# Kernel tuning notes

Measured on AMD Instinct MI355X. Metric: run time of the kernel, lower is better.

## Reference

```python
import jax, jax.numpy as jnp
import numpy as np

HID = 768        # config.hidden_size
MM_HID = 1024    # config.mmodal_hidden_size
N_Q = 64         # config.num_queries
WIN = 512        # config.window_size
LN_EPS = 1e-5


def _window_starts(m, n, w):
    # mirrors split_tensor's start-index logic (static, computed in numpy)
    step = max(1, (m - w) // (n - 1))
    starts = []
    for i in range(n):
        s = i * step
        if s + w > m:
            s = m - w
        starts.append(s)
    return np.asarray(starts, dtype=np.int32)


def layernorm(x, g, b):
    mu = jnp.mean(x, axis=-1, keepdims=True)
    var = jnp.var(x, axis=-1, keepdims=True)
    return (x - mu) * jax.lax.rsqrt(var + LN_EPS) * g + b


def setup_inputs() -> dict:
    key = jax.random.key(0)
    ks = jax.random.split(key, 12)
    b, m, li = 4, 8192, 77
    s = lambda fan_in: 1.0 / np.sqrt(fan_in)
    inp = {
        'x_mmodal': jax.random.normal(ks[0], (b, m, MM_HID), jnp.float32),
        'inst_feats': jax.random.normal(ks[1], (b, li, HID), jnp.float32),
        'queries': jax.random.normal(ks[2], (1, N_Q, HID), jnp.float32),
        'W_proj': jax.random.normal(ks[3], (HID, HID), jnp.float32) * s(HID),
        'b_proj': jnp.zeros((HID,), jnp.float32),
        'W_kv_inst': jax.random.normal(ks[4], (HID, 2 * HID), jnp.float32) * s(HID),
        'b_kv_inst': jnp.zeros((2 * HID,), jnp.float32),
        'W_out_inst': jax.random.normal(ks[5], (HID, HID), jnp.float32) * s(HID),
        'b_out_inst': jnp.zeros((HID,), jnp.float32),
        'W_kv_mm': jax.random.normal(ks[6], (MM_HID, 2 * HID), jnp.float32) * s(MM_HID),
        'b_kv_mm': jnp.zeros((2 * HID,), jnp.float32),
        'W_out_mm': jax.random.normal(ks[7], (HID, HID), jnp.float32) * s(HID),
        'b_out_mm': jnp.zeros((HID,), jnp.float32),
        'ln_g': jnp.ones((HID,), jnp.float32),
        'ln_b': jnp.zeros((HID,), jnp.float32),
    }
    return inp


def reference(x_mmodal, inst_feats, queries, W_proj, b_proj, W_kv_inst,
              b_kv_inst, W_out_inst, b_out_inst, W_kv_mm, b_kv_mm,
              W_out_mm, b_out_mm, ln_g, ln_b):
    b = x_mmodal.shape[0]
    scale = 1.0 / jnp.sqrt(jnp.asarray(HID, x_mmodal.dtype))

    # ---- dense cross-attention over instruction features ----
    inst = inst_feats @ W_proj + b_proj                      # (b, li, d)
    k, v = jnp.split(inst @ W_kv_inst + b_kv_inst, 2, axis=-1)
    k = layernorm(k, ln_g, ln_b)
    v = layernorm(v, ln_g, ln_b)
    q = jnp.broadcast_to(queries, (b, N_Q, HID))
    attn = jnp.einsum('bnd,bmd->bnm', q, k) * scale
    attn = jax.nn.softmax(attn, axis=-1)
    q = jnp.einsum('bnm,bmd->bnd', attn, v)
    q = layernorm(q @ W_out_inst + b_out_inst, ln_g, ln_b)

    # ---- swin-style overlapping windowed cross-attention over mmodal ----
    k, v = jnp.split(x_mmodal @ W_kv_mm + b_kv_mm, 2, axis=-1)
    k = layernorm(k, ln_g, ln_b)
    v = layernorm(v, ln_g, ln_b)
    m = k.shape[1]
    starts = _window_starts(m, N_Q, WIN)                     # (n,)
    idx = jnp.asarray(starts[:, None] + np.arange(WIN))      # (n, w)
    kw = k[:, idx]                                           # (b, n, w, d)
    vw = v[:, idx]                                           # (b, n, w, d)
    a = jnp.einsum('bnd,bnwd->bnw', q, kw) * scale
    a = jax.nn.softmax(a, axis=-1)
    out = jnp.einsum('bnw,bnwd->bnd', a, vw)
    out = layernorm(out @ W_out_mm + b_out_mm, ln_g, ln_b)
    return out
```

## Files before the change

### kernel.cpp

```cpp
#include <hip/hip_runtime.h>

#define HIDDEN 768
#define NQ 64
#define WINSZ 512
#define MSEQ 8192
#define BATCH 4
#define LI 77
#define MMHID 1024
#define LN_EPS 1e-5f
#define SCALE_QK 0.03608439182435161f

typedef __attribute__((ext_vector_type(8))) short short8v;
typedef __attribute__((ext_vector_type(4))) float f32x4;
typedef __attribute__((ext_vector_type(8))) unsigned short u16x8;

#define AS1 __attribute__((address_space(1)))
#define AS3 __attribute__((address_space(3)))

__device__ inline unsigned short f2bf(float f) {
    unsigned u = __float_as_uint(f);
    u += 0x7fffu + ((u >> 16) & 1u);
    return (unsigned short)(u >> 16);
}
__device__ inline float bf2f(unsigned short h) {
    return __uint_as_float(((unsigned)h) << 16);
}

__device__ inline void block_reduce2_256(float& s1, float& s2, float* sm) {
    #pragma unroll
    for (int o = 32; o; o >>= 1) { s1 += __shfl_down(s1, o); s2 += __shfl_down(s2, o); }
    int lane = threadIdx.x & 63, w = threadIdx.x >> 6;
    __syncthreads();
    if (lane == 0) { sm[w] = s1; sm[4 + w] = s2; }
    __syncthreads();
    s1 = sm[0] + sm[1] + sm[2] + sm[3];
    s2 = sm[4] + sm[5] + sm[6] + sm[7];
}

__global__ __launch_bounds__(256) void cvt_kernel(const float* __restrict__ in,
                                                  unsigned short* __restrict__ out, int n8) {
    int i = blockIdx.x * 256 + threadIdx.x;
    if (i >= n8) return;
    const float4* p = (const float4*)(in + (size_t)i * 8);
    float4 a = p[0], b = p[1];
    u16x8 o;
    o[0] = f2bf(a.x); o[1] = f2bf(a.y); o[2] = f2bf(a.z); o[3] = f2bf(a.w);
    o[4] = f2bf(b.x); o[5] = f2bf(b.y); o[6] = f2bf(b.z); o[7] = f2bf(b.w);
    *(u16x8*)(out + (size_t)i * 8) = o;
}

__global__ __launch_bounds__(256) void cvt_q_kernel(const float* __restrict__ q2,
                                                    const float* __restrict__ g,
                                                    const float* __restrict__ bb,
                                                    unsigned short* __restrict__ q2bf,
                                                    float* __restrict__ qgsum) {
    int blk = blockIdx.x;
    int b = blk >> 7, r = blk & 127;
    int t = threadIdx.x;
    __shared__ float sm[8];
    unsigned short* orow = q2bf + (size_t)blk * HIDDEN;
    if (r >= 64) {
        orow[t] = 0; orow[t + 256] = 0; orow[t + 512] = 0;
        return;
    }
    const float* qrow = q2 + ((size_t)(b * 64 + r)) * HIDDEN;
    float y0 = qrow[t], y1 = qrow[t + 256], y2 = qrow[t + 512];
    float s = y0 + y1 + y2, s2 = y0 * y0 + y1 * y1 + y2 * y2;
    block_reduce2_256(s, s2, sm);
    float mu = s * (1.f / 768.f);
    float var = s2 * (1.f / 768.f) - mu * mu;
    float inv = rsqrtf(var + LN_EPS);
    float qw0 = (y0 - mu) * inv * g[t]       + bb[t];
    float qw1 = (y1 - mu) * inv * g[t + 256] + bb[t + 256];
    float qw2 = (y2 - mu) * inv * g[t + 512] + bb[t + 512];
    float v0 = qw0 * g[t]       * SCALE_QK;
    float v1 = qw1 * g[t + 256] * SCALE_QK;
    float v2 = qw2 * g[t + 512] * SCALE_QK;
    orow[t] = f2bf(v0); orow[t + 256] = f2bf(v1); orow[t + 512] = f2bf(v2);
    float qs = v0 + v1 + v2, dummy = 0.f;
    block_reduce2_256(qs, dummy, sm);
    if (t == 0) qgsum[b * 64 + r] = qs;
}

struct PrepJobs {
    const float* W[5];
    unsigned short* Wt[5];
    int D[5];
    int C[5];
    const float* inst_in;
    unsigned short* inst_out;
    int n8_valid;
    int n8_total;
};
__global__ __launch_bounds__(256) void prep_kernel(PrepJobs tw) {
    int z = blockIdx.z;
    if (z == 5) {
        int flat = blockIdx.y * gridDim.x + blockIdx.x;
        int i = flat * 256 + threadIdx.x;
        if (i >= tw.n8_total) return;
        u16x8 o = {};
        if (i < tw.n8_valid) {
            const float4* p = (const float4*)(tw.inst_in + (size_t)i * 8);
            float4 a = p[0], b = p[1];
            o[0] = f2bf(a.x); o[1] = f2bf(a.y); o[2] = f2bf(a.z); o[3] = f2bf(a.w);
            o[4] = f2bf(b.x); o[5] = f2bf(b.y); o[6] = f2bf(b.z); o[7] = f2bf(b.w);
        }
        *(u16x8*)(tw.inst_out + (size_t)i * 8) = o;
        return;
    }
    int C = tw.C[z], D = tw.D[z];
    int n0 = blockIdx.x * 32, k0 = blockIdx.y * 32;
    if (n0 >= C || k0 >= D) return;
    const float* W = tw.W[z];
    unsigned short* Wt = tw.Wt[z];
    __shared__ float tile[32][33];
    int tx = threadIdx.x & 31, ty = (threadIdx.x >> 5);
    #pragma unroll
    for (int i = 0; i < 32; i += 8)
        tile[ty + i][tx] = W[(size_t)(k0 + ty + i) * C + n0 + tx];
    __syncthreads();
    #pragma unroll
    for (int i = 0; i < 32; i += 8)
        Wt[(size_t)(n0 + ty + i) * D + k0 + tx] = f2bf(tile[tx][ty + i]);
}

#define GM 32768
#define GN 1536
#define GK 1024

__global__ __launch_bounds__(256) void gemm_kv_kernel(const unsigned short* __restrict__ A,
                                                      const unsigned short* __restrict__ Bt,
                                                      const float* __restrict__ bias,
                                                      unsigned short* __restrict__ C) {
    __shared__ unsigned short sA[128 * 64];
    __shared__ unsigned short sB[128 * 64];

    int nwg = gridDim.x;
    int bid = blockIdx.x;
    int wg = bid;
    if ((nwg & 7) == 0) { int cpx = nwg >> 3; wg = (bid & 7) * cpx + (bid >> 3); }
    int bm = wg / (GN / 128), bn = wg % (GN / 128);
    int row0 = bm * 128, col0 = bn * 128;

    int tid = threadIdx.x;
    int lane = tid & 63, wid = tid >> 6;
    int wr = wid >> 1, wc = wid & 1;

    f32x4 acc[4][4] = {};

    int rS[4], cS[4];
    #pragma unroll
    for (int i = 0; i < 4; i++) {
        int ch = wid * 4 + i;
        int r = ch * 8 + (lane >> 3);
        rS[i] = r;
        cS[i] = ((lane & 7) ^ (r & 7)) << 3;
    }

    for (int k0 = 0; k0 < GK; k0 += 64) {
        #pragma unroll
        for (int i = 0; i < 4; i++) {
            int ch = wid * 4 + i;
            const unsigned short* ga = A + (size_t)(row0 + rS[i]) * GK + k0 + cS[i];
            __builtin_amdgcn_global_load_lds((const AS1 unsigned int*)ga,
                                             (AS3 unsigned int*)&sA[ch * 512], 16, 0, 0);
            const unsigned short* gb = Bt + (size_t)(col0 + rS[i]) * GK + k0 + cS[i];
            __builtin_amdgcn_global_load_lds((const AS1 unsigned int*)gb,
                                             (AS3 unsigned int*)&sB[ch * 512], 16, 0, 0);
        }
        __syncthreads();

        #pragma unroll
        for (int kk = 0; kk < 64; kk += 32) {
            int ko = (kk + ((lane >> 4) << 3)) * 2;
            short8v af[4], bf[4];
            #pragma unroll
            for (int m = 0; m < 4; m++) {
                int r = wr * 64 + m * 16 + (lane & 15);
                int addr = r * 128 + (ko ^ ((r & 7) << 4));
                af[m] = *(const short8v*)((const char*)sA + addr);
            }
            #pragma unroll
            for (int n = 0; n < 4; n++) {
                int r = wc * 64 + n * 16 + (lane & 15);
                int addr = r * 128 + (ko ^ ((r & 7) << 4));
                bf[n] = *(const short8v*)((const char*)sB + addr);
            }
            #pragma unroll
            for (int m = 0; m < 4; m++)
                #pragma unroll
                for (int n = 0; n < 4; n++)
                    acc[m][n] = __builtin_amdgcn_mfma_f32_16x16x32_bf16(af[m], bf[n], acc[m][n], 0, 0, 0);
        }
        __syncthreads();
    }

    int crow = (lane >> 4) * 4;
    int ccol = lane & 15;
    #pragma unroll
    for (int m = 0; m < 4; m++) {
        #pragma unroll
        for (int n = 0; n < 4; n++) {
            int gc = col0 + wc * 64 + n * 16 + ccol;
            float bv = bias[gc];
            #pragma unroll
            for (int j = 0; j < 4; j++) {
                int gr = row0 + wr * 64 + m * 16 + crow + j;
                C[(size_t)gr * GN + gc] = f2bf(acc[m][n][j] + bv);
            }
        }
    }
}

__global__ __launch_bounds__(256) void stats_kernel(const unsigned short* __restrict__ kv,
                                                    float2* __restrict__ stats) {
    int rh = blockIdx.x;
    const unsigned short* p = kv + (size_t)rh * 768;
    int t = threadIdx.x;
    float x0 = bf2f(p[t]), x1 = bf2f(p[t + 256]), x2 = bf2f(p[t + 512]);
    float s = x0 + x1 + x2, s2 = x0 * x0 + x1 * x1 + x2 * x2;
    __shared__ float sm[8];
    block_reduce2_256(s, s2, sm);
    if (t == 0) {
        float mu = s * (1.f / 768.f);
        float var = s2 * (1.f / 768.f) - mu * mu;
        float inv = rsqrtf(var + LN_EPS);
        stats[rh] = make_float2(mu * inv, inv);
    }
}

template <int TK, bool OUT_BF16>
__global__ __launch_bounds__(256) void gemm_tile_kernel(const unsigned short* __restrict__ A,
                                                        const unsigned short* __restrict__ Bt,
                                                        const float* __restrict__ bias,
                                                        void* __restrict__ Cout, int N) {
    __shared__ unsigned short sA[128 * 64];
    __shared__ unsigned short sB[128 * 64];

    int row0 = blockIdx.x * 128, col0 = blockIdx.y * 128;
    int tid = threadIdx.x;
    int lane = tid & 63, wid = tid >> 6;
    int wr = wid >> 1, wc = wid & 1;

    f32x4 acc[4][4] = {};

    int rS[4], cS[4];
    #pragma unroll
    for (int i = 0; i < 4; i++) {
        int ch = wid * 4 + i;
        int r = ch * 8 + (lane >> 3);
        rS[i] = r;
        cS[i] = ((lane & 7) ^ (r & 7)) << 3;
    }

    for (int k0 = 0; k0 < TK; k0 += 64) {
        #pragma unroll
        for (int i = 0; i < 4; i++) {
            int ch = wid * 4 + i;
            const unsigned short* ga = A + (size_t)(row0 + rS[i]) * TK + k0 + cS[i];
            __builtin_amdgcn_global_load_lds((const AS1 unsigned int*)ga,
                                             (AS3 unsigned int*)&sA[ch * 512], 16, 0, 0);
            const unsigned short* gb = Bt + (size_t)(col0 + rS[i]) * TK + k0 + cS[i];
            __builtin_amdgcn_global_load_lds((const AS1 unsigned int*)gb,
                                             (AS3 unsigned int*)&sB[ch * 512], 16, 0, 0);
        }
        __syncthreads();

        #pragma unroll
        for (int kk = 0; kk < 64; kk += 32) {
            int ko = (kk + ((lane >> 4) << 3)) * 2;
            short8v af[4], bf[4];
            #pragma unroll
            for (int m = 0; m < 4; m++) {
                int r = wr * 64 + m * 16 + (lane & 15);
                int addr = r * 128 + (ko ^ ((r & 7) << 4));
                af[m] = *(const short8v*)((const char*)sA + addr);
            }
            #pragma unroll
            for (int n = 0; n < 4; n++) {
                int r = wc * 64 + n * 16 + (lane & 15);
                int addr = r * 128 + (ko ^ ((r & 7) << 4));
                bf[n] = *(const short8v*)((const char*)sB + addr);
            }
            #pragma unroll
            for (int m = 0; m < 4; m++)
                #pragma unroll
                for (int n = 0; n < 4; n++)
                    acc[m][n] = __builtin_amdgcn_mfma_f32_16x16x32_bf16(af[m], bf[n], acc[m][n], 0, 0, 0);
        }
        __syncthreads();
    }

    int crow = (lane >> 4) * 4;
    int ccol = lane & 15;
    #pragma unroll
    for (int m = 0; m < 4; m++) {
        #pragma unroll
        for (int n = 0; n < 4; n++) {
            int gc = col0 + wc * 64 + n * 16 + ccol;
            float bv = bias[gc];
            #pragma unroll
            for (int j = 0; j < 4; j++) {
                int gr = row0 + wr * 64 + m * 16 + crow + j;
                float v = acc[m][n][j] + bv;
                if (OUT_BF16) ((unsigned short*)Cout)[(size_t)gr * N + gc] = f2bf(v);
                else          ((float*)Cout)[(size_t)gr * N + gc] = v;
            }
        }
    }
}

__global__ __launch_bounds__(256) void gemm_scores_kernel(const unsigned short* __restrict__ Aall,
                                                          const unsigned short* __restrict__ kv,
                                                          float* __restrict__ scores) {
    __shared__ unsigned short sA[128 * 64];
    __shared__ unsigned short sB[128 * 64];

    int b = blockIdx.y;
    int col0 = blockIdx.x * 128;
    const unsigned short* A = Aall + (size_t)b * 128 * HIDDEN;
    const unsigned short* Bt = kv + (size_t)b * MSEQ * 1536;

    int tid = threadIdx.x;
    int lane = tid & 63, wid = tid >> 6;
    int wr = wid >> 1, wc = wid & 1;

    f32x4 acc[4][4] = {};

    int rS[4], cS[4];
    #pragma unroll
    for (int i = 0; i < 4; i++) {
        int ch = wid * 4 + i;
        int r = ch * 8 + (lane >> 3);
        rS[i] = r;
        cS[i] = ((lane & 7) ^ (r & 7)) << 3;
    }

    for (int k0 = 0; k0 < HIDDEN; k0 += 64) {
        #pragma unroll
        for (int i = 0; i < 4; i++) {
            int ch = wid * 4 + i;
            const unsigned short* ga = A + (size_t)rS[i] * HIDDEN + k0 + cS[i];
            __builtin_amdgcn_global_load_lds((const AS1 unsigned int*)ga,
                                             (AS3 unsigned int*)&sA[ch * 512], 16, 0, 0);
            const unsigned short* gb = Bt + (size_t)(col0 + rS[i]) * 1536 + k0 + cS[i];
            __builtin_amdgcn_global_load_lds((const AS1 unsigned int*)gb,
                                             (AS3 unsigned int*)&sB[ch * 512], 16, 0, 0);
        }
        __syncthreads();

        #pragma unroll
        for (int kk = 0; kk < 64; kk += 32) {
            int ko = (kk + ((lane >> 4) << 3)) * 2;
            short8v af[4], bf[4];
            #pragma unroll
            for (int m = 0; m < 4; m++) {
                int r = wr * 64 + m * 16 + (lane & 15);
                int addr = r * 128 + (ko ^ ((r & 7) << 4));
                af[m] = *(const short8v*)((const char*)sA + addr);
            }
            #pragma unroll
            for (int n = 0; n < 4; n++) {
                int r = wc * 64 + n * 16 + (lane & 15);
                int addr = r * 128 + (ko ^ ((r & 7) << 4));
                bf[n] = *(const short8v*)((const char*)sB + addr);
            }
            #pragma unroll
            for (int m = 0; m < 4; m++)
                #pragma unroll
                for (int n = 0; n < 4; n++)
                    acc[m][n] = __builtin_amdgcn_mfma_f32_16x16x32_bf16(af[m], bf[n], acc[m][n], 0, 0, 0);
        }
        __syncthreads();
    }

    int crow = (lane >> 4) * 4;
    int ccol = lane & 15;
    #pragma unroll
    for (int m = 0; m < 4; m++) {
        #pragma unroll
        for (int n = 0; n < 4; n++) {
            int gc = col0 + wc * 64 + n * 16 + ccol;
            #pragma unroll
            for (int j = 0; j < 4; j++) {
                int gr = wr * 64 + m * 16 + crow + j;
                if (gr < 64)
                    scores[((size_t)(b * 64 + gr)) * MSEQ + gc] = acc[m][n][j];
            }
        }
    }
}

__global__ __launch_bounds__(512) void win_softmax_kernel(const float* __restrict__ scores,
                                                          const float2* __restrict__ stats,
                                                          const float* __restrict__ qgsum,
                                                          unsigned short* __restrict__ P_abs,
                                                          float* __restrict__ s2out) {
    int bidx = blockIdx.x;
    int b = bidx >> 6, n = bidx & 63;
    int step = (MSEQ - WINSZ) / (NQ - 1);
    int s = n * step;
    if (s + WINSZ > MSEQ) s = MSEQ - WINSZ;

    __shared__ float sm[8];
    int t = threadIdx.x, lane = t & 63, w = t >> 6;
    int r_abs = s + t;
    size_t rowidx = (size_t)b * MSEQ + r_abs;
    float2 stk = stats[rowidx * 2 + 0];
    float qg = qgsum[b * 64 + n];
    float a = stk.y * scores[((size_t)(b * 64 + n)) * MSEQ + r_abs] - qg * stk.x;

    float m = a;
    #pragma unroll
    for (int o = 32; o; o >>= 1) m = fmaxf(m, __shfl_down(m, o));
    if (lane == 0) sm[w] = m;
    __syncthreads();
    m = sm[0];
    #pragma unroll
    for (int i = 1; i < 8; i++) m = fmaxf(m, sm[i]);
    float e = expf(a - m);
    float ssum = e;
    #pragma unroll
    for (int o = 32; o; o >>= 1) ssum += __shfl_down(ssum, o);
    __syncthreads();
    if (lane == 0) sm[w] = ssum;
    __syncthreads();
    ssum = 0;
    #pragma unroll
    for (int i = 0; i < 8; i++) ssum += sm[i];
    float p = e / ssum;

    float2 stv = stats[rowidx * 2 + 1];
    float pt = p * stv.y;
    float s2p = p * stv.x;
    #pragma unroll
    for (int o = 32; o; o >>= 1) s2p += __shfl_down(s2p, o);
    __syncthreads();
    if (lane == 0) sm[w] = s2p;
    __syncthreads();
    if (t == 0) {
        float s2 = 0;
        #pragma unroll
        for (int i = 0; i < 8; i++) s2 += sm[i];
        s2out[b * 64 + n] = s2;
    }

    unsigned short* prow = P_abs + ((size_t)(b * 64 + n)) * MSEQ;
    for (int pos = t; pos < MSEQ; pos += 512)
        if (pos < s || pos >= s + WINSZ) prow[pos] = 0;
    prow[r_abs] = f2bf(pt);
}

__global__ __launch_bounds__(768) void pv_chunk_kernel(const unsigned short* __restrict__ P_abs,
                                                       const unsigned short* __restrict__ kv,
                                                       float* __restrict__ out_acc) {
    int b = blockIdx.y;
    int r0 = blockIdx.x * 64;
    int t = threadIdx.x;

    int n_lo = (r0 >= 512) ? ((r0 - 512) / 121 + 1) : 0;
    int n_hi = (r0 + 63) / 121;
    if (n_hi > 63) n_hi = 63;

    __shared__ float pw[5][64];
    if (t < 5 * 64) {
        int ni = t >> 6, r = t & 63;
        int n = n_lo + ni;
        float v = 0.f;
        if (n <= n_hi)
            v = bf2f(P_abs[((size_t)(b * 64 + n)) * MSEQ + r0 + r]);
        pw[ni][r] = v;
    }
    __syncthreads();

    const unsigned short* vbase = kv + ((size_t)(b * MSEQ + r0)) * 1536 + 768;
    float acc[5] = {};
    #pragma unroll 8
    for (int r = 0; r < 64; ++r) {
        float v = bf2f(vbase[(size_t)r * 1536 + t]);
        #pragma unroll
        for (int ni = 0; ni < 5; ni++) acc[ni] = fmaf(v, pw[ni][r], acc[ni]);
    }
    #pragma unroll
    for (int ni = 0; ni < 5; ni++) {
        int n = n_lo + ni;
        if (n <= n_hi)
            atomicAdd(&out_acc[((size_t)(b * 64 + n)) * HIDDEN + t], acc[ni]);
    }
}

__global__ __launch_bounds__(256) void out_affine_kernel(const float* __restrict__ o_acc,
                                                         const float* __restrict__ s2,
                                                         const float* __restrict__ g,
                                                         const float* __restrict__ bb,
                                                         unsigned short* __restrict__ a_bf) {
    int i = blockIdx.x * 256 + threadIdx.x;
    if (i >= BATCH * NQ * HIDDEN) return;
    int n = i / HIDDEN, d = i - n * HIDDEN;
    a_bf[i] = f2bf(g[d] * (o_acc[i] - s2[n]) + bb[d]);
}

__global__ __launch_bounds__(256) void ln_f32_rows(float* __restrict__ base,
                                                   const float* __restrict__ g,
                                                   const float* __restrict__ b) {
    int rh = blockIdx.x;
    float* p = base + (size_t)rh * 768;
    int t = threadIdx.x;
    float x0 = p[t], x1 = p[t + 256], x2 = p[t + 512];
    float s = x0 + x1 + x2, s2 = x0 * x0 + x1 * x1 + x2 * x2;
    __shared__ float sm[8];
    block_reduce2_256(s, s2, sm);
    float mu = s * (1.f / 768.f);
    float var = s2 * (1.f / 768.f) - mu * mu;
    float inv = rsqrtf(var + LN_EPS);
    p[t]       = (x0 - mu) * inv * g[t]       + b[t];
    p[t + 256] = (x1 - mu) * inv * g[t + 256] + b[t + 256];
    p[t + 512] = (x2 - mu) * inv * g[t + 512] + b[t + 512];
}

__global__ __launch_bounds__(256) void attn_inst_kernel(const float* __restrict__ queries,
                                                        const float* __restrict__ kv,
                                                        unsigned short* __restrict__ qatt) {
    int bidx = blockIdx.x;
    int b = bidx >> 6, n = bidx & 63;
    __shared__ float qs[HIDDEN];
    __shared__ float sc[LI], sc2[LI];
    int t = threadIdx.x, lane = t & 63, w = t >> 6;
    const float* q = queries + (size_t)n * HIDDEN;
    for (int d = t; d < HIDDEN; d += 256) qs[d] = q[d];
    __syncthreads();
    const float* kb = kv + (size_t)b * LI * 1536;
    for (int j = w; j < LI; j += 4) {
        const float* kr = kb + (size_t)j * 1536;
        float a = 0;
        #pragma unroll
        for (int i = 0; i < 12; i++) { int d = lane + i * 64; a = fmaf(kr[d], qs[d], a); }
        #pragma unroll
        for (int o = 32; o; o >>= 1) a += __shfl_down(a, o);
        if (lane == 0) sc[j] = a * SCALE_QK;
    }
    __syncthreads();
    float m = -1e30f;
    for (int j = 0; j < LI; j++) m = fmaxf(m, sc[j]);
    if (t < LI) sc2[t] = expf(sc[t] - m);
    __syncthreads();
    float s = 0;
    for (int j = 0; j < LI; j++) s += sc2[j];
    float inv = 1.f / s;
    float o0 = 0, o1 = 0, o2 = 0;
    for (int j = 0; j < LI; j++) {
        float p = sc2[j] * inv;
        const float* vr = kb + (size_t)j * 1536 + 768;
        o0 = fmaf(p, vr[t], o0);
        o1 = fmaf(p, vr[t + 256], o1);
        o2 = fmaf(p, vr[t + 512], o2);
    }
    unsigned short* orow = qatt + ((size_t)b * NQ + n) * HIDDEN;
    orow[t] = f2bf(o0); orow[t + 256] = f2bf(o1); orow[t + 512] = f2bf(o2);
}

extern "C" void kernel_launch(void* const* d_in, const int* in_sizes, int n_in,
                              void* d_out, int out_size, void* d_ws, size_t ws_size,
                              hipStream_t stream) {
    (void)in_sizes; (void)n_in; (void)out_size; (void)ws_size;
    const float* x_mm    = (const float*)d_in[0];
    const float* instf   = (const float*)d_in[1];
    const float* queries = (const float*)d_in[2];
    const float* W_proj  = (const float*)d_in[3];
    const float* b_proj  = (const float*)d_in[4];
    const float* W_kvi   = (const float*)d_in[5];
    const float* b_kvi   = (const float*)d_in[6];
    const float* W_oi    = (const float*)d_in[7];
    const float* b_oi    = (const float*)d_in[8];
    const float* W_kvm   = (const float*)d_in[9];
    const float* b_kvm   = (const float*)d_in[10];
    const float* W_om    = (const float*)d_in[11];
    const float* b_om    = (const float*)d_in[12];
    const float* ln_g    = (const float*)d_in[13];
    const float* ln_b    = (const float*)d_in[14];
    float* out = (float*)d_out;

    char* ws = (char*)d_ws;
    size_t off = 0;
    auto carve = [&](size_t bytes) -> char* {
        char* p = ws + off;
        off += (bytes + 255) & ~(size_t)255;
        return p;
    };
    unsigned short* x_bf   = (unsigned short*)carve((size_t)BATCH * MSEQ * MMHID * 2);
    unsigned short* wtm_bf = (unsigned short*)carve((size_t)2 * HIDDEN * MMHID * 2);
    unsigned short* kv_mm  = (unsigned short*)carve((size_t)BATCH * MSEQ * 2 * HIDDEN * 2);
    unsigned short* wp_bf  = (unsigned short*)carve((size_t)768 * 768 * 2);
    unsigned short* wkvi_bf= (unsigned short*)carve((size_t)1536 * 768 * 2);
    unsigned short* woi_bf = (unsigned short*)carve((size_t)768 * 768 * 2);
    unsigned short* wom_bf = (unsigned short*)carve((size_t)768 * 768 * 2);
    unsigned short* a1_bf  = (unsigned short*)carve((size_t)384 * 768 * 2);
    unsigned short* inst_bf= (unsigned short*)carve((size_t)384 * 768 * 2);
    float*          kv_inst= (float*)carve((size_t)384 * 1536 * 4);
    unsigned short* qatt_bf= (unsigned short*)carve((size_t)256 * 768 * 2);
    float*          q2     = (float*)carve((size_t)256 * 768 * 4);
    unsigned short* q2bf   = (unsigned short*)carve((size_t)BATCH * 128 * 768 * 2);
    float*          scores = (float*)carve((size_t)BATCH * 64 * MSEQ * 4);
    unsigned short* P_abs  = (unsigned short*)carve((size_t)BATCH * 64 * MSEQ * 2);
    float*          o_acc  = (float*)carve((size_t)BATCH * 64 * 768 * 4);
    unsigned short* a_bf   = (unsigned short*)carve((size_t)256 * 768 * 2);
    float2*         stats  = (float2*)carve((size_t)BATCH * MSEQ * 2 * sizeof(float2));
    float*          qgsum  = (float*)carve((size_t)256 * 4);
    float*          s2     = (float*)carve((size_t)256 * 4);

    PrepJobs tw;
    tw.W[0] = W_kvm;  tw.Wt[0] = wtm_bf;  tw.D[0] = 1024; tw.C[0] = 1536;
    tw.W[1] = W_proj; tw.Wt[1] = wp_bf;   tw.D[1] = 768;  tw.C[1] = 768;
    tw.W[2] = W_kvi;  tw.Wt[2] = wkvi_bf; tw.D[2] = 768;  tw.C[2] = 1536;
    tw.W[3] = W_oi;   tw.Wt[3] = woi_bf;  tw.D[3] = 768;  tw.C[3] = 768;
    tw.W[4] = W_om;   tw.Wt[4] = wom_bf;  tw.D[4] = 768;  tw.C[4] = 768;
    tw.inst_in = instf; tw.inst_out = a1_bf;
    tw.n8_valid = BATCH * LI * 768 / 8; tw.n8_total = 384 * 768 / 8;
    prep_kernel<<<dim3(48, 32, 6), 256, 0, stream>>>(tw);

    int n8 = BATCH * MSEQ * MMHID / 8;
    cvt_kernel<<<(n8 + 255) / 256, 256, 0, stream>>>(x_mm, x_bf, n8);
    gemm_kv_kernel<<<(GM / 128) * (GN / 128), 256, 0, stream>>>(x_bf, wtm_bf, b_kvm, kv_mm);
    stats_kernel<<<BATCH * MSEQ * 2, 256, 0, stream>>>(kv_mm, stats);

    gemm_tile_kernel<768, true><<<dim3(3, 6), 256, 0, stream>>>(a1_bf, wp_bf, b_proj, inst_bf, 768);
    gemm_tile_kernel<768, false><<<dim3(3, 12), 256, 0, stream>>>(inst_bf, wkvi_bf, b_kvi, kv_inst, 1536);
    ln_f32_rows<<<BATCH * LI * 2, 256, 0, stream>>>(kv_inst, ln_g, ln_b);
    attn_inst_kernel<<<BATCH * NQ, 256, 0, stream>>>(queries, kv_inst, qatt_bf);
    gemm_tile_kernel<768, false><<<dim3(2, 6), 256, 0, stream>>>(qatt_bf, woi_bf, b_oi, q2, 768);

    hipMemsetAsync(o_acc, 0, (size_t)BATCH * 64 * 768 * 4, stream);
    cvt_q_kernel<<<BATCH * 128, 256, 0, stream>>>(q2, ln_g, ln_b, q2bf, qgsum);
    gemm_scores_kernel<<<dim3(MSEQ / 128, BATCH), 256, 0, stream>>>(q2bf, kv_mm, scores);
    win_softmax_kernel<<<BATCH * NQ, 512, 0, stream>>>(scores, stats, qgsum, P_abs, s2);
    pv_chunk_kernel<<<dim3(MSEQ / 64, BATCH), 768, 0, stream>>>(P_abs, kv_mm, o_acc);
    out_affine_kernel<<<(BATCH * NQ * HIDDEN + 255) / 256, 256, 0, stream>>>(o_acc, s2, ln_g, ln_b, a_bf);

    gemm_tile_kernel<768, false><<<dim3(2, 6), 256, 0, stream>>>(a_bf, wom_bf, b_om, out, 768);
    ln_f32_rows<<<BATCH * NQ, 256, 0, stream>>>(out, ln_g, ln_b);
}
```

Baseline: 346.4 us.

## Use 256x256-tile double-buffered MFMA GEMM for multimodal KV projection

```diff
diff --git a/kernel.cpp b/kernel.cpp
--- a/kernel.cpp
+++ b/kernel.cpp
@@ -128,10 +128,116 @@
 #define GN 1536
 #define GK 1024
 
-__global__ __launch_bounds__(256) void gemm_kv_kernel(const unsigned short* __restrict__ A,
-                                                      const unsigned short* __restrict__ Bt,
-                                                      const float* __restrict__ bias,
-                                                      unsigned short* __restrict__ C) {
+__global__ __launch_bounds__(512, 2) void gemm_kv256_kernel(const unsigned short* __restrict__ A,
+                                                            const unsigned short* __restrict__ Bt,
+                                                            const float* __restrict__ bias,
+                                                            unsigned short* __restrict__ C) {
+    extern __shared__ char smem[];
+    unsigned short* sA = (unsigned short*)smem;
+    unsigned short* sB = (unsigned short*)(smem + 65536);
+
+    int nwg = gridDim.x;
+    int bid = blockIdx.x;
+    int wg = bid;
+    if ((nwg & 7) == 0) { int cpx = nwg >> 3; wg = (bid & 7) * cpx + (bid >> 3); }
+    int bm = wg / (GN / 256), bn = wg % (GN / 256);
+    int row0 = bm * 256, col0 = bn * 256;
+
+    int tid = threadIdx.x;
+    int lane = tid & 63, wid = tid >> 6;
+    int wm = wid >> 2, wn = wid & 3;
+
+    f32x4 acc[8][4] = {};
+
+    int rS[4], cS[4];
+    #pragma unroll
+    for (int i = 0; i < 4; i++) {
+        int ch = wid * 4 + i;
+        int r = ch * 8 + (lane >> 3);
+        rS[i] = r;
+        cS[i] = ((lane & 7) ^ (r & 7)) << 3;
+    }
+
+    auto STAGE = [&](int k0, int pbuf) {
+        unsigned short* dA = sA + pbuf * 16384;
+        unsigned short* dB = sB + pbuf * 16384;
+        #pragma unroll
+        for (int i = 0; i < 4; i++) {
+            int ch = wid * 4 + i;
+            const unsigned short* ga = A + (size_t)(row0 + rS[i]) * GK + k0 + cS[i];
+            __builtin_amdgcn_global_load_lds((const AS1 unsigned int*)ga,
+                                             (AS3 unsigned int*)&dA[ch * 512], 16, 0, 0);
+            const unsigned short* gb = Bt + (size_t)(col0 + rS[i]) * GK + k0 + cS[i];
+            __builtin_amdgcn_global_load_lds((const AS1 unsigned int*)gb,
+                                             (AS3 unsigned int*)&dB[ch * 512], 16, 0, 0);
+        }
+    };
+
+    STAGE(0, 0);
+    __syncthreads();
+
+    for (int kt = 0; kt < GK / 64; kt++) {
+        int cur = kt & 1;
+        if (kt < GK / 64 - 1) STAGE((kt + 1) * 64, cur ^ 1);
+
+        const char* lA = (const char*)(sA + cur * 16384);
+        const char* lB = (const char*)(sB + cur * 16384);
+
+        short8v bfr[4][2];
+        #pragma unroll
+        for (int n = 0; n < 4; n++)
+            #pragma unroll
+            for (int kk = 0; kk < 2; kk++) {
+                int r = wn * 64 + n * 16 + (lane & 15);
+                int ko = (kk * 32 + ((lane >> 4) << 3)) * 2;
+                bfr[n][kk] = *(const short8v*)(lB + r * 128 + (ko ^ ((r & 7) << 4)));
+            }
+        #pragma unroll
+        for (int p = 0; p < 4; p++) {
+            short8v afr[2][2];
+            #pragma unroll
+            for (int mf = 0; mf < 2; mf++)
+                #pragma unroll
+                for (int kk = 0; kk < 2; kk++) {
+                    int r = wm * 128 + (p * 2 + mf) * 16 + (lane & 15);
+                    int ko = (kk * 32 + ((lane >> 4) << 3)) * 2;
+                    afr[mf][kk] = *(const short8v*)(lA + r * 128 + (ko ^ ((r & 7) << 4)));
+                }
+            __builtin_amdgcn_s_setprio(1);
+            #pragma unroll
+            for (int mf = 0; mf < 2; mf++)
+                #pragma unroll
+                for (int n = 0; n < 4; n++)
+                    #pragma unroll
+                    for (int kk = 0; kk < 2; kk++)
+                        acc[p * 2 + mf][n] = __builtin_amdgcn_mfma_f32_16x16x32_bf16(
+                            afr[mf][kk], bfr[n][kk], acc[p * 2 + mf][n], 0, 0, 0);
+            __builtin_amdgcn_s_setprio(0);
+        }
+        __syncthreads();
+    }
+
+    int crow = (lane >> 4) * 4;
+    int ccol = lane & 15;
+    #pragma unroll
+    for (int m = 0; m < 8; m++) {
+        #pragma unroll
+        for (int n = 0; n < 4; n++) {
+            int gc = col0 + wn * 64 + n * 16 + ccol;
+            float bv = bias[gc];
+            #pragma unroll
+            for (int j = 0; j < 4; j++) {
+                int gr = row0 + wm * 128 + m * 16 + crow + j;
+                C[(size_t)gr * GN + gc] = f2bf(acc[m][n][j] + bv);
+            }
+        }
+    }
+}
+
+__global__ __launch_bounds__(256) void gemm_kv128_kernel(const unsigned short* __restrict__ A,
+                                                         const unsigned short* __restrict__ Bt,
+                                                         const float* __restrict__ bias,
+                                                         unsigned short* __restrict__ C) {
     __shared__ unsigned short sA[128 * 64];
     __shared__ unsigned short sB[128 * 64];
 
@@ -620,7 +726,13 @@
 
     int n8 = BATCH * MSEQ * MMHID / 8;
     cvt_kernel<<<(n8 + 255) / 256, 256, 0, stream>>>(x_mm, x_bf, n8);
-    gemm_kv_kernel<<<(GM / 128) * (GN / 128), 256, 0, stream>>>(x_bf, wtm_bf, b_kvm, kv_mm);
+    hipError_t attr_ok = hipFuncSetAttribute((const void*)gemm_kv256_kernel,
+                                             hipFuncAttributeMaxDynamicSharedMemorySize, 131072);
+    if (attr_ok == hipSuccess) {
+        gemm_kv256_kernel<<<(GM / 256) * (GN / 256), 512, 131072, stream>>>(x_bf, wtm_bf, b_kvm, kv_mm);
+    } else {
+        gemm_kv128_kernel<<<(GM / 128) * (GN / 128), 256, 0, stream>>>(x_bf, wtm_bf, b_kvm, kv_mm);
+    }
     stats_kernel<<<BATCH * MSEQ * 2, 256, 0, stream>>>(kv_mm, stats);
 
     gemm_tile_kernel<768, true><<<dim3(3, 6), 256, 0, stream>>>(a1_bf, wp_bf, b_proj, inst_bf, 768);
```

Result: faster. 320.3 us (-7.6%).

## Double-buffer KV GEMM with 256x128 tiles and fold o_acc zeroing into softmax

Applied to the files above, without the earlier changes.

```diff
diff --git a/kernel.cpp b/kernel.cpp
--- a/kernel.cpp
+++ b/kernel.cpp
@@ -128,69 +128,94 @@
 #define GN 1536
 #define GK 1024
 
-__global__ __launch_bounds__(256) void gemm_kv_kernel(const unsigned short* __restrict__ A,
-                                                      const unsigned short* __restrict__ Bt,
-                                                      const float* __restrict__ bias,
-                                                      unsigned short* __restrict__ C) {
-    __shared__ unsigned short sA[128 * 64];
-    __shared__ unsigned short sB[128 * 64];
+__global__ __launch_bounds__(256, 2) void gemm_kv_kernel(const unsigned short* __restrict__ A,
+                                                         const unsigned short* __restrict__ Bt,
+                                                         const float* __restrict__ bias,
+                                                         unsigned short* __restrict__ C) {
+    __shared__ unsigned short sA[2][256 * 32];
+    __shared__ unsigned short sB[2][128 * 32];
 
     int nwg = gridDim.x;
     int bid = blockIdx.x;
     int wg = bid;
     if ((nwg & 7) == 0) { int cpx = nwg >> 3; wg = (bid & 7) * cpx + (bid >> 3); }
     int bm = wg / (GN / 128), bn = wg % (GN / 128);
-    int row0 = bm * 128, col0 = bn * 128;
+    int row0 = bm * 256, col0 = bn * 128;
 
     int tid = threadIdx.x;
     int lane = tid & 63, wid = tid >> 6;
-    int wr = wid >> 1, wc = wid & 1;
-
-    f32x4 acc[4][4] = {};
-
-    int rS[4], cS[4];
+    int wm = wid >> 1, wn = wid & 1;
+
+    f32x4 acc[8][4] = {};
+
+    int rA[4], cA[4];
     #pragma unroll
     for (int i = 0; i < 4; i++) {
         int ch = wid * 4 + i;
-        int r = ch * 8 + (lane >> 3);
-        rS[i] = r;
-        cS[i] = ((lane & 7) ^ (r & 7)) << 3;
-    }
-
-    for (int k0 = 0; k0 < GK; k0 += 64) {
+        int r = ch * 16 + (lane >> 2);
+        rA[i] = r;
+        cA[i] = ((((lane & 3) * 16) ^ ((r & 6) << 3)) >> 1);
+    }
+    int rB[2], cB[2];
+    #pragma unroll
+    for (int i = 0; i < 2; i++) {
+        int ch = wid * 2 + i;
+        int r = ch * 16 + (lane >> 2);
+        rB[i] = r;
+        cB[i] = ((((lane & 3) * 16) ^ ((r & 6) << 3)) >> 1);
+    }
+
+    auto STAGE = [&](int k0, int pbuf) {
         #pragma unroll
         for (int i = 0; i < 4; i++) {
             int ch = wid * 4 + i;
-            const unsigned short* ga = A + (size_t)(row0 + rS[i]) * GK + k0 + cS[i];
+            const unsigned short* ga = A + (size_t)(row0 + rA[i]) * GK + k0 + cA[i];
             __builtin_amdgcn_global_load_lds((const AS1 unsigned int*)ga,
-                                             (AS3 unsigned int*)&sA[ch * 512], 16, 0, 0);
-            const unsigned short* gb = Bt + (size_t)(col0 + rS[i]) * GK + k0 + cS[i];
+                                             (AS3 unsigned int*)&sA[pbuf][ch * 512], 16, 0, 0);
+        }
+        #pragma unroll
+        for (int i = 0; i < 2; i++) {
+            int ch = wid * 2 + i;
+            const unsigned short* gb = Bt + (size_t)(col0 + rB[i]) * GK + k0 + cB[i];
             __builtin_amdgcn_global_load_lds((const AS1 unsigned int*)gb,
-                                             (AS3 unsigned int*)&sB[ch * 512], 16, 0, 0);
-        }
-        __syncthreads();
-
-        #pragma unroll
-        for (int kk = 0; kk < 64; kk += 32) {
-            int ko = (kk + ((lane >> 4) << 3)) * 2;
-            short8v af[4], bf[4];
-            #pragma unroll
-            for (int m = 0; m < 4; m++) {
-                int r = wr * 64 + m * 16 + (lane & 15);
-                int addr = r * 128 + (ko ^ ((r & 7) << 4));
-                af[m] = *(const short8v*)((const char*)sA + addr);
-            }
-            #pragma unroll
-            for (int n = 0; n < 4; n++) {
-                int r = wc * 64 + n * 16 + (lane & 15);
-                int addr = r * 128 + (ko ^ ((r & 7) << 4));
-                bf[n] = *(const short8v*)((const char*)sB + addr);
-            }
-            #pragma unroll
-            for (int m = 0; m < 4; m++)
+                                             (AS3 unsigned int*)&sB[pbuf][ch * 512], 16, 0, 0);
+        }
+    };
+
+    STAGE(0, 0);
+    __syncthreads();
+
+    int kob = (lane >> 4) * 16;
+
+    for (int kt = 0; kt < GK / 32; kt++) {
+        int cur = kt & 1;
+        if (kt < GK / 32 - 1) STAGE((kt + 1) * 32, cur ^ 1);
+
+        const char* lA = (const char*)sA[cur];
+        const char* lB = (const char*)sB[cur];
+
+        short8v bfr[4];
+        #pragma unroll
+        for (int n = 0; n < 4; n++) {
+            int r = wn * 64 + n * 16 + (lane & 15);
+            bfr[n] = *(const short8v*)(lB + r * 64 + (kob ^ ((r & 6) << 3)));
+        }
+        #pragma unroll
+        for (int p = 0; p < 4; p++) {
+            short8v afr[2];
+            #pragma unroll
+            for (int mf = 0; mf < 2; mf++) {
+                int r = wm * 128 + (p * 2 + mf) * 16 + (lane & 15);
+                afr[mf] = *(const short8v*)(lA + r * 64 + (kob ^ ((r & 6) << 3)));
+            }
+            __builtin_amdgcn_s_setprio(1);
+            #pragma unroll
+            for (int mf = 0; mf < 2; mf++)
                 #pragma unroll
                 for (int n = 0; n < 4; n++)
-                    acc[m][n] = __builtin_amdgcn_mfma_f32_16x16x32_bf16(af[m], bf[n], acc[m][n], 0, 0, 0);
+                    acc[p * 2 + mf][n] = __builtin_amdgcn_mfma_f32_16x16x32_bf16(
+                        afr[mf], bfr[n], acc[p * 2 + mf][n], 0, 0, 0);
+            __builtin_amdgcn_s_setprio(0);
         }
         __syncthreads();
     }
@@ -198,14 +223,14 @@
     int crow = (lane >> 4) * 4;
     int ccol = lane & 15;
     #pragma unroll
-    for (int m = 0; m < 4; m++) {
+    for (int m = 0; m < 8; m++) {
         #pragma unroll
         for (int n = 0; n < 4; n++) {
-            int gc = col0 + wc * 64 + n * 16 + ccol;
+            int gc = col0 + wn * 64 + n * 16 + ccol;
             float bv = bias[gc];
             #pragma unroll
             for (int j = 0; j < 4; j++) {
-                int gr = row0 + wr * 64 + m * 16 + crow + j;
+                int gr = row0 + wm * 128 + m * 16 + crow + j;
                 C[(size_t)gr * GN + gc] = f2bf(acc[m][n][j] + bv);
             }
         }
@@ -395,7 +420,8 @@
                                                           const float2* __restrict__ stats,
                                                           const float* __restrict__ qgsum,
                                                           unsigned short* __restrict__ P_abs,
-                                                          float* __restrict__ s2out) {
+                                                          float* __restrict__ s2out,
+                                                          float* __restrict__ o_acc) {
     int bidx = blockIdx.x;
     int b = bidx >> 6, n = bidx & 63;
     int step = (MSEQ - WINSZ) / (NQ - 1);
@@ -404,6 +430,11 @@
 
     __shared__ float sm[8];
     int t = threadIdx.x, lane = t & 63, w = t >> 6;
+
+    float* oz = o_acc + ((size_t)(b * 64 + n)) * HIDDEN;
+    oz[t] = 0.f;
+    if (t < 256) oz[512 + t] = 0.f;
+
     int r_abs = s + t;
     size_t rowidx = (size_t)b * MSEQ + r_abs;
     float2 stk = stats[rowidx * 2 + 0];
@@ -620,7 +651,7 @@
 
     int n8 = BATCH * MSEQ * MMHID / 8;
     cvt_kernel<<<(n8 + 255) / 256, 256, 0, stream>>>(x_mm, x_bf, n8);
-    gemm_kv_kernel<<<(GM / 128) * (GN / 128), 256, 0, stream>>>(x_bf, wtm_bf, b_kvm, kv_mm);
+    gemm_kv_kernel<<<(GM / 256) * (GN / 128), 256, 0, stream>>>(x_bf, wtm_bf, b_kvm, kv_mm);
     stats_kernel<<<BATCH * MSEQ * 2, 256, 0, stream>>>(kv_mm, stats);
 
     gemm_tile_kernel<768, true><<<dim3(3, 6), 256, 0, stream>>>(a1_bf, wp_bf, b_proj, inst_bf, 768);
@@ -629,10 +660,9 @@
     attn_inst_kernel<<<BATCH * NQ, 256, 0, stream>>>(queries, kv_inst, qatt_bf);
     gemm_tile_kernel<768, false><<<dim3(2, 6), 256, 0, stream>>>(qatt_bf, woi_bf, b_oi, q2, 768);
 
-    hipMemsetAsync(o_acc, 0, (size_t)BATCH * 64 * 768 * 4, stream);
     cvt_q_kernel<<<BATCH * 128, 256, 0, stream>>>(q2, ln_g, ln_b, q2bf, qgsum);
     gemm_scores_kernel<<<dim3(MSEQ / 128, BATCH), 256, 0, stream>>>(q2bf, kv_mm, scores);
-    win_softmax_kernel<<<BATCH * NQ, 512, 0, stream>>>(scores, stats, qgsum, P_abs, s2);
+    win_softmax_kernel<<<BATCH * NQ, 512, 0, stream>>>(scores, stats, qgsum, P_abs, s2, o_acc);
     pv_chunk_kernel<<<dim3(MSEQ / 64, BATCH), 768, 0, stream>>>(P_abs, kv_mm, o_acc);
     out_affine_kernel<<<(BATCH * NQ * HIDDEN + 255) / 256, 256, 0, stream>>>(o_acc, s2, ln_g, ln_b, a_bf);
 
```

Result: faster. 331.4 us (-4.3%).
